# Optimization experiments

Hardware: AMD Instinct MI355X
Metric: run time of the kernel (lower is better)

## Reference

```python
import jax, jax.numpy as jnp
import numpy as np

Q_WINDOW = 2  # matches init kwarg Q


def setup_inputs() -> dict:
    key = jax.random.key(0)
    k1, k2, k3 = jax.random.split(key, 3)
    B, M, D, C = 32, 2048, 1024, 5
    embeds_x = jax.random.normal(k1, (B, M, D), jnp.float32)
    embeds_y = jax.random.normal(k2, (B, C * D, 1), jnp.float32)
    # small scale on P keeps the bilinear logits in a sane softmax range
    P = jax.random.normal(k3, (D, C * D), jnp.float32) * 1e-3
    return {"embeds_x": embeds_x, "embeds_y": embeds_y, "P": P, "M": M}


def reference(embeds_x, embeds_y, P, M):
    # embeds_x: [B, M, D], embeds_y: [B, C*D, 1], P: [D, C*D]
    B, Mx, D = embeds_x.shape
    Q = Q_WINDOW

    # Sliding-window sums via cumsum (replaces the per-timestep Python loop).
    # Original torch code: x_bar[:, i, :] = sum(x[:, s:e, :]) / Q with
    # s = max(i-Q, 0), e = min(i+Q, M-1), slice end EXCLUSIVE, built from .data
    # (i.e. detached from autograd).
    cs = jnp.concatenate(
        [jnp.zeros((B, 1, D), embeds_x.dtype), jnp.cumsum(embeds_x, axis=1)], axis=1
    )  # [B, M+1, D]
    i = jnp.arange(M)
    s = jnp.clip(i - Q, 0, None)
    e = jnp.clip(i + Q, None, M - 1)
    x_bar = (cs[:, e, :] - cs[:, s, :]) / Q  # [B, M, D]
    x_bar = jax.lax.stop_gradient(x_bar)

    # Bilinear attention scores: a = P @ y, p = x @ a
    a = jnp.einsum('dk,bko->bdo', P, embeds_y)          # [B, D, 1]
    logits = jnp.einsum('bmd,bdo->bmo', embeds_x, a)    # [B, M, 1]
    # legacy F.softmax on [M, B, 1] -> dim 0, i.e. softmax over sequence M
    p = jax.nn.softmax(logits, axis=1)                  # [B, M, 1]

    # enc = (x_bar^T @ p).squeeze : weighted sum of smoothed embeddings
    enc = jnp.einsum('bmd,bmo->bd', x_bar, p)           # [B, D]
    return enc
```

## Files before the change

### kernel.cpp

```cpp
#include <hip/hip_runtime.h>

#define BB 32
#define MM 2048
#define DD 1024
#define KK 5120

#define R3 16
#define NCH 128

__global__ __launch_bounds__(256) void k_a(const float* __restrict__ P,
                                           const float* __restrict__ y,
                                           float* __restrict__ a) {
    const int d0 = blockIdx.x * 4;
    const int wave = threadIdx.x >> 6;
    const int lane = threadIdx.x & 63;
    const int b0 = wave * 8;

    float acc[4][8];
#pragma unroll
    for (int i = 0; i < 4; ++i)
#pragma unroll
        for (int j = 0; j < 8; ++j) acc[i][j] = 0.f;

    for (int i = 0; i < 20; ++i) {
        const int k4 = lane + i * 64;
        float4 pv[4], yv[8];
#pragma unroll
        for (int dd = 0; dd < 4; ++dd)
            pv[dd] = ((const float4*)(P + (size_t)(d0 + dd) * KK))[k4];
#pragma unroll
        for (int bb = 0; bb < 8; ++bb)
            yv[bb] = ((const float4*)(y + (size_t)(b0 + bb) * KK))[k4];
#pragma unroll
        for (int dd = 0; dd < 4; ++dd)
#pragma unroll
            for (int bb = 0; bb < 8; ++bb) {
                acc[dd][bb] = fmaf(pv[dd].x, yv[bb].x, acc[dd][bb]);
                acc[dd][bb] = fmaf(pv[dd].y, yv[bb].y, acc[dd][bb]);
                acc[dd][bb] = fmaf(pv[dd].z, yv[bb].z, acc[dd][bb]);
                acc[dd][bb] = fmaf(pv[dd].w, yv[bb].w, acc[dd][bb]);
            }
    }

#pragma unroll
    for (int dd = 0; dd < 4; ++dd)
#pragma unroll
        for (int bb = 0; bb < 8; ++bb) {
            float v = acc[dd][bb];
#pragma unroll
            for (int off = 32; off; off >>= 1) v += __shfl_xor(v, off, 64);
            if (lane == 0) a[(size_t)(b0 + bb) * DD + (d0 + dd)] = v;
        }
}

__global__ __launch_bounds__(256) void k_fused3(const float* __restrict__ x,
                                                const float* __restrict__ a,
                                                float* __restrict__ part,
                                                float* __restrict__ Spart) {
    const int w = threadIdx.x >> 6;
    const int lane = threadIdx.x & 63;
    const int g = blockIdx.x * 4 + w;
    const int b = g >> 7;
    const int chunk = g & (NCH - 1);
    const int j0 = chunk * R3;

    const float4* a4 = (const float4*)(a + (size_t)b * DD);
    float4 av[4];
#pragma unroll
    for (int q = 0; q < 4; ++q) av[q] = a4[lane + 64 * q];

    const float* xb = x + (size_t)b * MM * DD;

    float4 xr[4][4];
    float er[4] = {0.f, 0.f, 0.f, 0.f};
    float4 acc[4];
#pragma unroll
    for (int q = 0; q < 4; ++q) acc[q] = make_float4(0.f, 0.f, 0.f, 0.f);
    float se = 0.f;

#pragma unroll
    for (int it = 0; it < R3 + 3; ++it) {
        const int m = j0 - 1 + it;
        const bool vm = (m >= 0) && (m < MM);
        const int s0 = it & 3;

        if (vm) {
            const float4* row4 = (const float4*)(xb + (size_t)m * DD);
#pragma unroll
            for (int q = 0; q < 4; ++q) xr[s0][q] = row4[lane + 64 * q];
        } else {
#pragma unroll
            for (int q = 0; q < 4; ++q) xr[s0][q] = make_float4(0.f, 0.f, 0.f, 0.f);
        }

        float s = 0.f;
#pragma unroll
        for (int q = 0; q < 4; ++q) {
            s = fmaf(xr[s0][q].x, av[q].x, s);
            s = fmaf(xr[s0][q].y, av[q].y, s);
            s = fmaf(xr[s0][q].z, av[q].z, s);
            s = fmaf(xr[s0][q].w, av[q].w, s);
        }
#pragma unroll
        for (int off = 32; off; off >>= 1) s += __shfl_xor(s, off, 64);
        const float e = vm ? __expf(s) : 0.f;
        er[s0] = e;

        if (it >= 1 && it < R3 + 1) se += e;

        if (it >= 3) {
            const int j = j0 - 3 + it;
            if (j != MM - 1) {
                const float c = er[0] + er[1] + er[2] + er[3];
                const int sj = (it + 2) & 3;
#pragma unroll
                for (int q = 0; q < 4; ++q) {
                    acc[q].x = fmaf(c, xr[sj][q].x, acc[q].x);
                    acc[q].y = fmaf(c, xr[sj][q].y, acc[q].y);
                    acc[q].z = fmaf(c, xr[sj][q].z, acc[q].z);
                    acc[q].w = fmaf(c, xr[sj][q].w, acc[q].w);
                }
            }
        }
    }

    float4* p4 = (float4*)part + (size_t)(b * NCH + chunk) * 256;
#pragma unroll
    for (int q = 0; q < 4; ++q) p4[lane + 64 * q] = acc[q];
    if (lane == 0) Spart[b * NCH + chunk] = se;
}

__global__ __launch_bounds__(256) void k_combine3(const float* __restrict__ part,
                                                  const float* __restrict__ Spart,
                                                  float* __restrict__ out) {
    const int b = blockIdx.y;
    const int sl = blockIdx.x;
    const int t = threadIdx.x;
    const int col = t & 31;
    const int grp = t >> 5;

    __shared__ float Ssh;
    __shared__ float4 red[8][32];

    if (t < 64) {
        float s = Spart[b * NCH + t] + Spart[b * NCH + 64 + t];
#pragma unroll
        for (int off = 32; off; off >>= 1) s += __shfl_xor(s, off, 64);
        if (t == 0) Ssh = s;
    }

    float4 acc = make_float4(0.f, 0.f, 0.f, 0.f);
    const float4* p4 = (const float4*)part + (size_t)b * NCH * 256 + sl * 32 + col;
    for (int c = grp; c < NCH; c += 8) {
        const float4 v = p4[(size_t)c * 256];
        acc.x += v.x; acc.y += v.y; acc.z += v.z; acc.w += v.w;
    }
    red[grp][col] = acc;
    __syncthreads();

    if (t < 32) {
        float4 s = red[0][t];
#pragma unroll
        for (int g2 = 1; g2 < 8; ++g2) {
            const float4 v = red[g2][t];
            s.x += v.x; s.y += v.y; s.z += v.z; s.w += v.w;
        }
        const float invS = 0.5f / Ssh;
        ((float4*)(out + (size_t)b * DD))[sl * 32 + t] =
            make_float4(s.x * invS, s.y * invS, s.z * invS, s.w * invS);
    }
}

__global__ __launch_bounds__(256) void k_logits(const float* __restrict__ x,
                                                const float* __restrict__ a,
                                                float* __restrict__ logits) {
    const int b = blockIdx.y;
    const int wave = threadIdx.x >> 6;
    const int lane = threadIdx.x & 63;
    const int m = blockIdx.x * 8 + wave * 2;
    const float* ab = a + (size_t)b * DD;
    const float* row0 = x + ((size_t)b * MM + m) * DD;
    const float* row1 = row0 + DD;
    float s0 = 0.f, s1 = 0.f;
#pragma unroll
    for (int q = 0; q < 4; ++q) {
        const int d = lane * 4 + q * 256;
        const float4 av = *(const float4*)(ab + d);
        const float4 x0 = *(const float4*)(row0 + d);
        const float4 x1 = *(const float4*)(row1 + d);
        s0 = fmaf(x0.x, av.x, s0); s0 = fmaf(x0.y, av.y, s0);
        s0 = fmaf(x0.z, av.z, s0); s0 = fmaf(x0.w, av.w, s0);
        s1 = fmaf(x1.x, av.x, s1); s1 = fmaf(x1.y, av.y, s1);
        s1 = fmaf(x1.z, av.z, s1); s1 = fmaf(x1.w, av.w, s1);
    }
#pragma unroll
    for (int off = 32; off; off >>= 1) {
        s0 += __shfl_xor(s0, off, 64);
        s1 += __shfl_xor(s1, off, 64);
    }
    if (lane == 0) {
        logits[(size_t)b * MM + m] = s0;
        logits[(size_t)b * MM + m + 1] = s1;
    }
}

__global__ __launch_bounds__(256) void k_softmax_w(const float* __restrict__ logits,
                                                   float* __restrict__ w) {
    const int b = blockIdx.x;
    __shared__ float p[MM];
    __shared__ float red[8];
    const int t = threadIdx.x;
    const int lane = t & 63, wave = t >> 6;
    float mx = -INFINITY;
    for (int m = t; m < MM; m += 256) {
        const float v = logits[(size_t)b * MM + m];
        p[m] = v;
        mx = fmaxf(mx, v);
    }
#pragma unroll
    for (int off = 32; off; off >>= 1) mx = fmaxf(mx, __shfl_xor(mx, off, 64));
    if (lane == 0) red[wave] = mx;
    __syncthreads();
    mx = fmaxf(fmaxf(red[0], red[1]), fmaxf(red[2], red[3]));
    float s = 0.f;
    for (int m = t; m < MM; m += 256) {
        const float e = __expf(p[m] - mx);
        p[m] = e;
        s += e;
    }
#pragma unroll
    for (int off = 32; off; off >>= 1) s += __shfl_xor(s, off, 64);
    if (lane == 0) red[4 + wave] = s;
    __syncthreads();
    s = red[4] + red[5] + red[6] + red[7];
    const float inv = 0.5f / s;
    for (int j = t; j < MM; j += 256) {
        float wv;
        if (j == MM - 1) wv = 0.f;
        else {
            float acc = p[j];
            if (j >= 1) acc += p[j - 1];
            if (j + 1 <= MM - 1) acc += p[j + 1];
            if (j + 2 <= MM - 1) acc += p[j + 2];
            wv = acc * inv;
        }
        w[(size_t)b * MM + j] = wv;
    }
}

__global__ void k_zero(float* __restrict__ out) {
    out[blockIdx.x * 256 + threadIdx.x] = 0.f;
}

__global__ __launch_bounds__(256) void k_enc(const float* __restrict__ x,
                                             const float* __restrict__ w,
                                             float* __restrict__ out) {
    const int b = (BB - 1) - blockIdx.y;
    const int chunk = 31 - blockIdx.x;
    const int j0 = chunk * (MM / 32);
    const int d = threadIdx.x * 4;
    float4 acc0 = {0.f, 0.f, 0.f, 0.f};
    float4 acc1 = {0.f, 0.f, 0.f, 0.f};
    const float* xb = x + (size_t)b * MM * DD + d;
    const float* wb = w + (size_t)b * MM;
    for (int j = j0 + (MM / 32) - 1; j >= j0; j -= 2) {
        const float w0 = wb[j];
        const float w1 = wb[j - 1];
        const float4 x0 = *(const float4*)(xb + (size_t)j * DD);
        const float4 x1 = *(const float4*)(xb + (size_t)(j - 1) * DD);
        acc0.x = fmaf(w0, x0.x, acc0.x); acc0.y = fmaf(w0, x0.y, acc0.y);
        acc0.z = fmaf(w0, x0.z, acc0.z); acc0.w = fmaf(w0, x0.w, acc0.w);
        acc1.x = fmaf(w1, x1.x, acc1.x); acc1.y = fmaf(w1, x1.y, acc1.y);
        acc1.z = fmaf(w1, x1.z, acc1.z); acc1.w = fmaf(w1, x1.w, acc1.w);
    }
    float* o = out + (size_t)b * DD + d;
    atomicAdd(o + 0, acc0.x + acc1.x);
    atomicAdd(o + 1, acc0.y + acc1.y);
    atomicAdd(o + 2, acc0.z + acc1.z);
    atomicAdd(o + 3, acc0.w + acc1.w);
}

extern "C" void kernel_launch(void* const* d_in, const int* in_sizes, int n_in,
                              void* d_out, int out_size, void* d_ws, size_t ws_size,
                              hipStream_t stream) {
    (void)in_sizes; (void)n_in; (void)out_size;
    const float* x = (const float*)d_in[0];
    const float* y = (const float*)d_in[1];
    const float* P = (const float*)d_in[2];
    float* out = (float*)d_out;

    float* ws = (float*)d_ws;
    float* a = ws;
    const size_t part_f = (size_t)BB * NCH * DD;
    const size_t need = (32768 + part_f + BB * NCH) * sizeof(float);

    k_a<<<dim3(DD / 4), dim3(256), 0, stream>>>(P, y, a);

    if (ws_size >= need) {
        float* part = ws + 32768;
        float* Spart = part + part_f;
        k_fused3<<<dim3(BB * NCH / 4), dim3(256), 0, stream>>>(x, a, part, Spart);
        k_combine3<<<dim3(8, BB), dim3(256), 0, stream>>>(part, Spart, out);
    } else {
        float* logits = ws + 32768;
        float* w = ws + 32768 + 65536;
        k_logits<<<dim3(MM / 8, BB), dim3(256), 0, stream>>>(x, a, logits);
        k_softmax_w<<<dim3(BB), dim3(256), 0, stream>>>(logits, w);
        k_zero<<<dim3((BB * DD) / 256), dim3(256), 0, stream>>>(out);
        k_enc<<<dim3(32, BB), dim3(256), 0, stream>>>(x, w, out);
    }
}
```

Before: 93.00 us.

## Software-pipeline fused kernel with double-buffered row groups and batched reductions

Rewrites the fused logits/softmax/window kernel as a manually unrolled pipeline. Two register banks of four rows each alternate, so loads for the next four rows are issued while the current group is being processed. The four row dot-product wave reductions are interleaved to shorten the dependency chain, and launch_bounds now requests two blocks per CU. The extra live float4 registers (32 row vectors) raise register pressure and can cause spills under the new occupancy bound.

```diff
diff --git a/kernel.cpp b/kernel.cpp
--- a/kernel.cpp
+++ b/kernel.cpp
@@ -53,10 +53,10 @@
         }
 }
 
-__global__ __launch_bounds__(256) void k_fused3(const float* __restrict__ x,
-                                                const float* __restrict__ a,
-                                                float* __restrict__ part,
-                                                float* __restrict__ Spart) {
+__global__ __launch_bounds__(256, 2) void k_fused4(const float* __restrict__ x,
+                                                   const float* __restrict__ a,
+                                                   float* __restrict__ part,
+                                                   float* __restrict__ Spart) {
     const int w = threadIdx.x >> 6;
     const int lane = threadIdx.x & 63;
     const int g = blockIdx.x * 4 + w;
@@ -65,68 +65,156 @@
     const int j0 = chunk * R3;
 
     const float4* a4 = (const float4*)(a + (size_t)b * DD);
-    float4 av[4];
-#pragma unroll
-    for (int q = 0; q < 4; ++q) av[q] = a4[lane + 64 * q];
+    const float4 av0 = a4[lane];
+    const float4 av1 = a4[lane + 64];
+    const float4 av2 = a4[lane + 128];
+    const float4 av3 = a4[lane + 192];
 
     const float* xb = x + (size_t)b * MM * DD;
-
-    float4 xr[4][4];
-    float er[4] = {0.f, 0.f, 0.f, 0.f};
-    float4 acc[4];
-#pragma unroll
-    for (int q = 0; q < 4; ++q) acc[q] = make_float4(0.f, 0.f, 0.f, 0.f);
-    float se = 0.f;
-
-#pragma unroll
-    for (int it = 0; it < R3 + 3; ++it) {
-        const int m = j0 - 1 + it;
-        const bool vm = (m >= 0) && (m < MM);
-        const int s0 = it & 3;
-
-        if (vm) {
-            const float4* row4 = (const float4*)(xb + (size_t)m * DD);
-#pragma unroll
-            for (int q = 0; q < 4; ++q) xr[s0][q] = row4[lane + 64 * q];
-        } else {
-#pragma unroll
-            for (int q = 0; q < 4; ++q) xr[s0][q] = make_float4(0.f, 0.f, 0.f, 0.f);
-        }
-
-        float s = 0.f;
-#pragma unroll
-        for (int q = 0; q < 4; ++q) {
-            s = fmaf(xr[s0][q].x, av[q].x, s);
-            s = fmaf(xr[s0][q].y, av[q].y, s);
-            s = fmaf(xr[s0][q].z, av[q].z, s);
-            s = fmaf(xr[s0][q].w, av[q].w, s);
-        }
-#pragma unroll
-        for (int off = 32; off; off >>= 1) s += __shfl_xor(s, off, 64);
-        const float e = vm ? __expf(s) : 0.f;
-        er[s0] = e;
-
-        if (it >= 1 && it < R3 + 1) se += e;
-
-        if (it >= 3) {
-            const int j = j0 - 3 + it;
-            if (j != MM - 1) {
-                const float c = er[0] + er[1] + er[2] + er[3];
-                const int sj = (it + 2) & 3;
-#pragma unroll
-                for (int q = 0; q < 4; ++q) {
-                    acc[q].x = fmaf(c, xr[sj][q].x, acc[q].x);
-                    acc[q].y = fmaf(c, xr[sj][q].y, acc[q].y);
-                    acc[q].z = fmaf(c, xr[sj][q].z, acc[q].z);
-                    acc[q].w = fmaf(c, xr[sj][q].w, acc[q].w);
-                }
-            }
-        }
-    }
+    const float4 fz = make_float4(0.f, 0.f, 0.f, 0.f);
+
+    float4 A00, A01, A02, A03, A10, A11, A12, A13;
+    float4 A20, A21, A22, A23, A30, A31, A32, A33;
+    float4 B00, B01, B02, B03, B10, B11, B12, B13;
+    float4 B20, B21, B22, B23, B30, B31, B32, B33;
+    float4 acc0 = fz, acc1 = fz, acc2 = fz, acc3 = fz;
+    float P0, P1, P2, P3, C0, C1, C2, C3, se = 0.f;
+    float s0, s1, s2, s3;
+
+#define LDROW(D0, D1, D2, D3, M, COND)                                        \
+    if (COND) {                                                               \
+        const float4* r4_ = (const float4*)(xb + (size_t)(M) * DD);           \
+        D0 = r4_[lane]; D1 = r4_[lane + 64];                                  \
+        D2 = r4_[lane + 128]; D3 = r4_[lane + 192];                           \
+    } else { D0 = fz; D1 = fz; D2 = fz; D3 = fz; }
+
+#define DOT16(S, R0, R1, R2, R3)                                              \
+    S = 0.f;                                                                  \
+    S = fmaf(R0.x, av0.x, S); S = fmaf(R0.y, av0.y, S);                       \
+    S = fmaf(R0.z, av0.z, S); S = fmaf(R0.w, av0.w, S);                       \
+    S = fmaf(R1.x, av1.x, S); S = fmaf(R1.y, av1.y, S);                       \
+    S = fmaf(R1.z, av1.z, S); S = fmaf(R1.w, av1.w, S);                       \
+    S = fmaf(R2.x, av2.x, S); S = fmaf(R2.y, av2.y, S);                       \
+    S = fmaf(R2.z, av2.z, S); S = fmaf(R2.w, av2.w, S);                       \
+    S = fmaf(R3.x, av3.x, S); S = fmaf(R3.y, av3.y, S);                       \
+    S = fmaf(R3.z, av3.z, S); S = fmaf(R3.w, av3.w, S);
+
+#define RED4()                                                                \
+    _Pragma("unroll")                                                         \
+    for (int off = 32; off; off >>= 1) {                                      \
+        s0 += __shfl_xor(s0, off, 64); s1 += __shfl_xor(s1, off, 64);         \
+        s2 += __shfl_xor(s2, off, 64); s3 += __shfl_xor(s3, off, 64);         \
+    }
+
+#define WIN(CC, X0, X1, X2, X3)                                               \
+    acc0.x = fmaf(CC, X0.x, acc0.x); acc0.y = fmaf(CC, X0.y, acc0.y);         \
+    acc0.z = fmaf(CC, X0.z, acc0.z); acc0.w = fmaf(CC, X0.w, acc0.w);         \
+    acc1.x = fmaf(CC, X1.x, acc1.x); acc1.y = fmaf(CC, X1.y, acc1.y);         \
+    acc1.z = fmaf(CC, X1.z, acc1.z); acc1.w = fmaf(CC, X1.w, acc1.w);         \
+    acc2.x = fmaf(CC, X2.x, acc2.x); acc2.y = fmaf(CC, X2.y, acc2.y);         \
+    acc2.z = fmaf(CC, X2.z, acc2.z); acc2.w = fmaf(CC, X2.w, acc2.w);         \
+    acc3.x = fmaf(CC, X3.x, acc3.x); acc3.y = fmaf(CC, X3.y, acc3.y);         \
+    acc3.z = fmaf(CC, X3.z, acc3.z); acc3.w = fmaf(CC, X3.w, acc3.w);
+
+    LDROW(A00, A01, A02, A03, j0 - 1, j0 > 0)
+    LDROW(A10, A11, A12, A13, j0 + 0, true)
+    LDROW(A20, A21, A22, A23, j0 + 1, true)
+    LDROW(A30, A31, A32, A33, j0 + 2, true)
+    LDROW(B00, B01, B02, B03, j0 + 3, true)
+    LDROW(B10, B11, B12, B13, j0 + 4, true)
+    LDROW(B20, B21, B22, B23, j0 + 5, true)
+    LDROW(B30, B31, B32, B33, j0 + 6, true)
+
+    DOT16(s0, A00, A01, A02, A03)
+    DOT16(s1, A10, A11, A12, A13)
+    DOT16(s2, A20, A21, A22, A23)
+    DOT16(s3, A30, A31, A32, A33)
+    RED4()
+    C0 = (j0 > 0) ? __expf(s0) : 0.f;
+    C1 = __expf(s1); C2 = __expf(s2); C3 = __expf(s3);
+    se += C1 + C2 + C3;
+    { const float c = C0 + C1 + C2 + C3; WIN(c, A10, A11, A12, A13) }
+    P0 = C0; P1 = C1; P2 = C2; P3 = C3;
+
+    DOT16(s0, B00, B01, B02, B03)
+    DOT16(s1, B10, B11, B12, B13)
+    DOT16(s2, B20, B21, B22, B23)
+    DOT16(s3, B30, B31, B32, B33)
+    RED4()
+    C0 = __expf(s0); C1 = __expf(s1); C2 = __expf(s2); C3 = __expf(s3);
+    se += C0 + C1 + C2 + C3;
+    { const float c = P1 + P2 + P3 + C0; WIN(c, A20, A21, A22, A23) }
+    { const float c = P2 + P3 + C0 + C1; WIN(c, A30, A31, A32, A33) }
+    LDROW(A00, A01, A02, A03, j0 + 7, true)
+    LDROW(A10, A11, A12, A13, j0 + 8, true)
+    LDROW(A20, A21, A22, A23, j0 + 9, true)
+    LDROW(A30, A31, A32, A33, j0 + 10, true)
+    { const float c = P3 + C0 + C1 + C2; WIN(c, B00, B01, B02, B03) }
+    { const float c = C0 + C1 + C2 + C3; WIN(c, B10, B11, B12, B13) }
+    P0 = C0; P1 = C1; P2 = C2; P3 = C3;
+
+    DOT16(s0, A00, A01, A02, A03)
+    DOT16(s1, A10, A11, A12, A13)
+    DOT16(s2, A20, A21, A22, A23)
+    DOT16(s3, A30, A31, A32, A33)
+    RED4()
+    C0 = __expf(s0); C1 = __expf(s1); C2 = __expf(s2); C3 = __expf(s3);
+    se += C0 + C1 + C2 + C3;
+    { const float c = P1 + P2 + P3 + C0; WIN(c, B20, B21, B22, B23) }
+    { const float c = P2 + P3 + C0 + C1; WIN(c, B30, B31, B32, B33) }
+    LDROW(B00, B01, B02, B03, j0 + 11, true)
+    LDROW(B10, B11, B12, B13, j0 + 12, true)
+    LDROW(B20, B21, B22, B23, j0 + 13, true)
+    LDROW(B30, B31, B32, B33, j0 + 14, true)
+    { const float c = P3 + C0 + C1 + C2; WIN(c, A00, A01, A02, A03) }
+    { const float c = C0 + C1 + C2 + C3; WIN(c, A10, A11, A12, A13) }
+    P0 = C0; P1 = C1; P2 = C2; P3 = C3;
+
+    DOT16(s0, B00, B01, B02, B03)
+    DOT16(s1, B10, B11, B12, B13)
+    DOT16(s2, B20, B21, B22, B23)
+    DOT16(s3, B30, B31, B32, B33)
+    RED4()
+    C0 = __expf(s0); C1 = __expf(s1); C2 = __expf(s2); C3 = __expf(s3);
+    se += C0 + C1 + C2 + C3;
+    { const float c = P1 + P2 + P3 + C0; WIN(c, A20, A21, A22, A23) }
+    { const float c = P2 + P3 + C0 + C1; WIN(c, A30, A31, A32, A33) }
+    LDROW(A00, A01, A02, A03, j0 + 15, true)
+    LDROW(A10, A11, A12, A13, j0 + 16, j0 + 16 < MM)
+    LDROW(A20, A21, A22, A23, j0 + 17, j0 + 17 < MM)
+    LDROW(A30, A31, A32, A33, 0, false)
+    { const float c = P3 + C0 + C1 + C2; WIN(c, B00, B01, B02, B03) }
+    { const float c = C0 + C1 + C2 + C3; WIN(c, B10, B11, B12, B13) }
+    P0 = C0; P1 = C1; P2 = C2; P3 = C3;
+
+    DOT16(s0, A00, A01, A02, A03)
+    DOT16(s1, A10, A11, A12, A13)
+    DOT16(s2, A20, A21, A22, A23)
+    DOT16(s3, A30, A31, A32, A33)
+    RED4()
+    C0 = __expf(s0);
+    C1 = (j0 + 16 < MM) ? __expf(s1) : 0.f;
+    C2 = (j0 + 17 < MM) ? __expf(s2) : 0.f;
+    C3 = 0.f;
+    se += C0;
+    { const float c = P1 + P2 + P3 + C0; WIN(c, B20, B21, B22, B23) }
+    { const float c = P2 + P3 + C0 + C1; WIN(c, B30, B31, B32, B33) }
+    {
+        float c = P3 + C0 + C1 + C2;
+        if (j0 + 15 == MM - 1) c = 0.f;
+        WIN(c, A00, A01, A02, A03)
+    }
+
+#undef LDROW
+#undef DOT16
+#undef RED4
+#undef WIN
 
     float4* p4 = (float4*)part + (size_t)(b * NCH + chunk) * 256;
-#pragma unroll
-    for (int q = 0; q < 4; ++q) p4[lane + 64 * q] = acc[q];
+    p4[lane] = acc0;
+    p4[lane + 64] = acc1;
+    p4[lane + 128] = acc2;
+    p4[lane + 192] = acc3;
     if (lane == 0) Spart[b * NCH + chunk] = se;
 }
 
@@ -299,7 +387,7 @@
     if (ws_size >= need) {
         float* part = ws + 32768;
         float* Spart = part + part_f;
-        k_fused3<<<dim3(BB * NCH / 4), dim3(256), 0, stream>>>(x, a, part, Spart);
+        k_fused4<<<dim3(BB * NCH / 4), dim3(256), 0, stream>>>(x, a, part, Spart);
         k_combine3<<<dim3(8, BB), dim3(256), 0, stream>>>(part, Spart, out);
     } else {
         float* logits = ws + 32768;
```

New measurement: 133.7 us. 43.7% more time.
